# Kernel optimization log

Hardware: AMD Instinct MI355X
Metric: run time of the kernel (lower is better)

## Reference

```python
import jax, jax.numpy as jnp
import numpy as np

B = 4096        # batch_size
D = 256         # feature_dim
N = 9000000     # dataset size (state buffer length)
G = 100         # num_groups
ALPHA = 0.5     # alpha_weight
GAMMA = 0.8
RHO = 8.0
LAM = 1.0       # lambada
ETA_P = 0.01
EPS = 1e-14
CLIP = 5.0


def setup_inputs() -> dict:
    key = jax.random.key(0)
    k = jax.random.split(key, 6)
    zis = jax.random.normal(k[0], (B, D), jnp.float32)
    zjs = jax.random.normal(k[1], (B, D), jnp.float32)
    # per-sample learned temperatures, small positive values
    taus_I = 0.01 + 0.2 * jax.random.uniform(k[2], (N,), jnp.float32)
    taus_T = 0.01 + 0.2 * jax.random.uniform(k[3], (N,), jnp.float32)
    group_info_I = jax.random.randint(k[4], (N,), 0, G, dtype=jnp.int32)
    group_info_T = jax.random.randint(k[5], (N,), 0, G, dtype=jnp.int32)
    ids = jnp.arange(B, dtype=jnp.int32)  # unique sample indices
    zeros_N = jnp.zeros((N,), jnp.float32)
    return {
        "zis": zis, "zjs": zjs,
        "s_I": zeros_N, "s_T": zeros_N, "b_I": zeros_N, "b_T": zeros_N,
        "z_I": jnp.zeros((G,), jnp.float32), "z_T": jnp.zeros((G,), jnp.float32),
        "p_I": jnp.ones((G,), jnp.float32) / G, "p_T": jnp.ones((G,), jnp.float32) / G,
        "taus_I": taus_I, "taus_T": taus_T,
        "ids": ids, "group_info_I": group_info_I, "group_info_T": group_info_T,
    }


def _l2norm(x):
    return x / jnp.maximum(jnp.linalg.norm(x, axis=1, keepdims=True), 1e-12)


def reference(zis, zjs, s_I, s_T, b_I, b_T, z_I, z_T, p_I, p_T,
              taus_I, taus_T, ids, group_info_I, group_info_T):
    zis = _l2norm(zis)
    zjs = _l2norm(zjs)
    sim = zis @ zjs.T                                   # [B, B]
    diag = jnp.diagonal(sim)                            # [B]
    mask_neg = 1.0 - jnp.eye(B, dtype=sim.dtype)
    image_diffs = sim - diag[:, None]
    text_diffs = sim - diag[None, :]

    tau_I = taus_I[ids]                                 # [B]
    tau_T = taus_T[ids]
    idt = jax.lax.stop_gradient(image_diffs / tau_I[:, None])
    tdt = jax.lax.stop_gradient(text_diffs / tau_T[None, :])

    # running max state (numerically-stable exp)
    old_b_I = b_I[ids]
    b_I_new = jnp.maximum(jnp.max(idt, axis=1), old_b_I)    # [B]
    old_b_T = b_T[ids]
    b_T_new = jnp.maximum(jnp.max(tdt, axis=0), old_b_T)    # [B]
    b_I = b_I.at[ids].set(b_I_new)
    b_T = b_T.at[ids].set(b_T_new)

    exp_I = jnp.exp(idt - b_I_new[:, None]) * mask_neg
    exp_T = jnp.exp(tdt - b_T_new[None, :]) * mask_neg
    g_I = jnp.sum(exp_I, axis=1)                         # [B]
    g_T = jnp.sum(exp_T, axis=0)                         # [B]

    # EMA of softmax denominators with max-rescaling
    s_I_new = (1.0 - GAMMA) * s_I[ids] * jnp.exp(old_b_I - b_I_new) + GAMMA * g_I
    s_T_new = (1.0 - GAMMA) * s_T[ids] * jnp.exp(old_b_T - b_T_new) + GAMMA * g_T
    s_I = s_I.at[ids].set(s_I_new)
    s_T = s_T.at[ids].set(s_T_new)
    s_I_c = jnp.maximum(s_I_new, EPS)
    s_T_c = jnp.maximum(s_T_new, EPS)

    w_I = exp_I / s_I_c[:, None]
    w_T = exp_T / s_T_c[None, :]

    gid_I = group_info_I[ids]                            # [B]
    gid_T = group_info_T[ids]
    gw_I = G * p_I[gid_I]                                # [B]
    gw_T = G * p_T[gid_T]

    image_loss = jnp.sum(w_I * gw_I[:, None] * image_diffs, axis=1)   # [B]
    text_loss = jnp.sum(w_T * gw_T[None, :] * text_diffs, axis=0)     # [B]
    total_loss = ALPHA * image_loss.mean() + (1.0 - ALPHA) * text_loss.mean()

    # per-group adversarial weight update
    F_I = tau_I * (jnp.log(s_I_c) + b_I_new + RHO)       # [B]
    F_T = tau_T * (jnp.log(s_T_c) + b_T_new + RHO)
    ones_b = jnp.ones((B,), sim.dtype)
    cnt_I = jnp.maximum(jax.ops.segment_sum(ones_b, gid_I, num_segments=G), 1.0)
    cnt_T = jnp.maximum(jax.ops.segment_sum(ones_b, gid_T, num_segments=G), 1.0)
    grad_p_I = jax.ops.segment_sum(F_I, gid_I, num_segments=G) / cnt_I
    grad_p_T = jax.ops.segment_sum(F_T, gid_T, num_segments=G) / cnt_T

    z_I = (1.0 - GAMMA) * z_I + GAMMA * grad_p_I
    z_T = (1.0 - GAMMA) * z_T + GAMMA * grad_p_T
    grad_hp_I = -LAM * jnp.log(p_I + EPS) - LAM
    grad_hp_T = -LAM * jnp.log(p_T + EPS) - LAM
    new_p_I = p_I * jnp.exp(2.0 * ETA_P * jnp.clip(z_I + grad_hp_I, -CLIP, CLIP))
    new_p_T = p_T * jnp.exp(2.0 * ETA_P * jnp.clip(z_T + grad_hp_T, -CLIP, CLIP))
    p_I = new_p_I / new_p_I.sum()
    p_T = new_p_T / new_p_T.sum()

    return total_loss, p_I, p_T
```

## Files before the change

kernel.cpp:

```cpp
#include <hip/hip_runtime.h>
#include <hip/hip_bf16.h>
#include <math.h>

#define BB 4096
#define DD 256
#define GG 100
#define GAMMA_C 0.8f
#define RHO_C 8.0f
#define ALPHA_C 0.5f
#define EPS_C 1e-14f
#define NSR 64
#define NSC 32

typedef __bf16 bf16x8 __attribute__((ext_vector_type(8)));
typedef float f32x16 __attribute__((ext_vector_type(16)));

__device__ inline int swzLoc(int r31, int k) {
    return ((k >> 4) << 9) | (((((k >> 3) & 1) << 5) | r31) << 3) | (k & 7);
}

__device__ inline float blockReduceSum(float v, float* lds) {
    for (int o = 32; o > 0; o >>= 1) v += __shfl_down(v, o);
    int lane = threadIdx.x & 63, wid = threadIdx.x >> 6;
    if (lane == 0) lds[wid] = v;
    __syncthreads();
    if (threadIdx.x == 0) {
        float r = lds[0];
        int nw = blockDim.x >> 6;
        for (int w = 1; w < nw; w++) r += lds[w];
        lds[0] = r;
    }
    __syncthreads();
    float r = lds[0];
    __syncthreads();
    return r;
}

__global__ void __launch_bounds__(256) norm_kernel(const float* __restrict__ zis,
                            const float* __restrict__ zjs,
                            ushort* __restrict__ zhi, ushort* __restrict__ zlo,
                            ushort* __restrict__ whi, ushort* __restrict__ wlo,
                            float* __restrict__ diag, float* __restrict__ acc) {
    __shared__ ushort st[4][8192];
    int rb = blockIdx.x;
    int wv = threadIdx.x >> 6, lane = threadIdx.x & 63;
    if (rb == 0) { acc[threadIdx.x] = 0.f; acc[threadIdx.x + 256] = 0.f; }
    for (int rr = 0; rr < 8; rr++) {
        int r = rb * 32 + wv * 8 + rr;
        float4 zv = *(const float4*)&zis[r * DD + lane * 4];
        float4 wv4 = *(const float4*)&zjs[r * DD + lane * 4];
        float sz = zv.x * zv.x + zv.y * zv.y + zv.z * zv.z + zv.w * zv.w;
        float sw = wv4.x * wv4.x + wv4.y * wv4.y + wv4.z * wv4.z + wv4.w * wv4.w;
        float dt = zv.x * wv4.x + zv.y * wv4.y + zv.z * wv4.z + zv.w * wv4.w;
        for (int mask = 1; mask <= 32; mask <<= 1) {
            sz += __shfl_xor(sz, mask);
            sw += __shfl_xor(sw, mask);
            dt += __shfl_xor(dt, mask);
        }
        float iz = 1.0f / fmaxf(sqrtf(sz), 1e-12f);
        float iw = 1.0f / fmaxf(sqrtf(sw), 1e-12f);
        if (lane == 0) diag[r] = dt * iz * iw;
        float nz[4] = {zv.x * iz, zv.y * iz, zv.z * iz, zv.w * iz};
        float nw[4] = {wv4.x * iw, wv4.y * iw, wv4.z * iw, wv4.w * iw};
        int r31 = wv * 8 + rr;
        for (int e = 0; e < 4; e++) {
            int k = lane * 4 + e;
            int li = swzLoc(r31, k);
            __hip_bfloat16 hz = __float2bfloat16(nz[e]);
            __hip_bfloat16 lz = __float2bfloat16(nz[e] - __bfloat162float(hz));
            __hip_bfloat16 hw = __float2bfloat16(nw[e]);
            __hip_bfloat16 lw = __float2bfloat16(nw[e] - __bfloat162float(hw));
            st[0][li] = *(ushort*)&hz;
            st[1][li] = *(ushort*)&lz;
            st[2][li] = *(ushort*)&hw;
            st[3][li] = *(ushort*)&lw;
        }
    }
    __syncthreads();
    size_t base = (size_t)rb * 8192;
    ushort* dsts[4] = {zhi + base, zlo + base, whi + base, wlo + base};
    for (int a = 0; a < 4; a++) {
        uint4* d = (uint4*)dsts[a];
        const uint4* s = (const uint4*)st[a];
        for (int it = 0; it < 4; it++) {
            int idx = it * 256 + threadIdx.x;
            d[idx] = s[idx];
        }
    }
}

__global__ void __launch_bounds__(256, 4) fused_tile(const ushort* __restrict__ Ahi,
        const ushort* __restrict__ Alo, const ushort* __restrict__ Bhi,
        const ushort* __restrict__ Blo, const float* __restrict__ diag,
        const float* __restrict__ tausI, const float* __restrict__ tausT,
        const int* __restrict__ ids,
        float* __restrict__ pmR, float* __restrict__ pgR, float* __restrict__ pwR,
        float* __restrict__ pmC, float* __restrict__ pgC, float* __restrict__ pwC) {
    __shared__ float rDiag[128], rITau[128];
    __shared__ float cDiag[64], cITau[64];
    __shared__ float cmS[4][64], cgS[4][64], cwS[4][64];
    __shared__ float tr[4][32 * 65];

    int lane = threadIdx.x & 63;
    int wv = threadIdx.x >> 6;
    int bm = blockIdx.y * 128, bn = blockIdx.x * 64;
    int h = lane >> 5, cl = lane & 31;

    if (threadIdx.x < 128) {
        int r = bm + threadIdx.x;
        rDiag[threadIdx.x] = diag[r];
        rITau[threadIdx.x] = 1.0f / tausI[ids[r]];
    } else if (threadIdx.x < 192) {
        int c = bn + threadIdx.x - 128;
        cDiag[threadIdx.x - 128] = diag[c];
        cITau[threadIdx.x - 128] = 1.0f / tausT[ids[c]];
    }

    int aBase = (blockIdx.y * 4 + wv) * 8192;
    int b0 = (blockIdx.x * 2) * 8192;
    int b1 = b0 + 8192;
    int lofs = lane * 8;

    f32x16 acc[2] = {};
#pragma unroll
    for (int s = 0; s < 16; s++) {
        int so = s * 512 + lofs;
        bf16x8 ah  = *(const bf16x8*)&Ahi[aBase + so];
        bf16x8 al  = *(const bf16x8*)&Alo[aBase + so];
        bf16x8 bh0 = *(const bf16x8*)&Bhi[b0 + so];
        bf16x8 bl0 = *(const bf16x8*)&Blo[b0 + so];
        bf16x8 bh1 = *(const bf16x8*)&Bhi[b1 + so];
        bf16x8 bl1 = *(const bf16x8*)&Blo[b1 + so];
        acc[0] = __builtin_amdgcn_mfma_f32_32x32x16_bf16(ah, bh0, acc[0], 0, 0, 0);
        acc[1] = __builtin_amdgcn_mfma_f32_32x32x16_bf16(ah, bh1, acc[1], 0, 0, 0);
        acc[0] = __builtin_amdgcn_mfma_f32_32x32x16_bf16(ah, bl0, acc[0], 0, 0, 0);
        acc[1] = __builtin_amdgcn_mfma_f32_32x32x16_bf16(ah, bl1, acc[1], 0, 0, 0);
        acc[0] = __builtin_amdgcn_mfma_f32_32x32x16_bf16(al, bh0, acc[0], 0, 0, 0);
        acc[1] = __builtin_amdgcn_mfma_f32_32x32x16_bf16(al, bh1, acc[1], 0, 0, 0);
    }

    __syncthreads();
    float cd2[2], cit2[2], cbloc[2], cg[2] = {}, cw[2] = {};
#pragma unroll
    for (int u = 0; u < 2; u++) {
        int clc = u * 32 + cl;
        cd2[u] = cDiag[clc];
        cit2[u] = cITau[clc];
        float m = -INFINITY;
#pragma unroll
        for (int reg = 0; reg < 16; reg++) m = fmaxf(m, acc[u][reg]);
        m = fmaxf(m, __shfl_xor(m, 32));
        cbloc[u] = (m - cd2[u]) * cit2[u];
    }
#pragma unroll
    for (int u = 0; u < 2; u++) {
        int gc = bn + u * 32 + cl;
#pragma unroll
        for (int reg = 0; reg < 16; reg++) {
            int gr = bm + wv * 32 + (reg & 3) + 4 * h + 8 * (reg >> 2);
            float v = acc[u][reg];
            bool off = gr != gc;
            float dvT = v - cd2[u];
            float eT = off ? __expf(dvT * cit2[u] - cbloc[u]) : 0.f;
            cg[u] += eT;
            cw[u] += eT * dvT;
        }
    }
#pragma unroll
    for (int u = 0; u < 2; u++) {
        cg[u] += __shfl_xor(cg[u], 32);
        cw[u] += __shfl_xor(cw[u], 32);
        if (h == 0) {
            cmS[wv][u * 32 + cl] = cbloc[u];
            cgS[wv][u * 32 + cl] = cg[u];
            cwS[wv][u * 32 + cl] = cw[u];
        }
    }

#pragma unroll
    for (int u = 0; u < 2; u++)
#pragma unroll
        for (int reg = 0; reg < 16; reg++) {
            int r = (reg & 3) + 4 * h + 8 * (reg >> 2);
            tr[wv][r * 65 + u * 32 + cl] = acc[u][reg];
        }
    __syncthreads();

    if (threadIdx.x < 64) {
        int c = threadIdx.x;
        float m = fmaxf(fmaxf(cmS[0][c], cmS[1][c]), fmaxf(cmS[2][c], cmS[3][c]));
        float g = 0.f, w = 0.f;
        for (int wq = 0; wq < 4; wq++) {
            float f = __expf(cmS[wq][c] - m);
            g += cgS[wq][c] * f;
            w += cwS[wq][c] * f;
        }
        size_t o = (size_t)blockIdx.y * BB + bn + c;
        pmC[o] = m;
        pgC[o] = g;
        pwC[o] = w;
    }

    {
        int r = cl;
        int grow = bm + wv * 32 + r;
        float rd = rDiag[wv * 32 + r];
        float rit = rITau[wv * 32 + r];
        float vv[32];
#pragma unroll
        for (int j = 0; j < 32; j++) vv[j] = tr[wv][r * 65 + h * 32 + j];
        float m = -INFINITY;
#pragma unroll
        for (int j = 0; j < 32; j++) m = fmaxf(m, vv[j]);
        m = fmaxf(m, __shfl_xor(m, 32));
        float bloc = (m - rd) * rit;
        float rg = 0.f, rw = 0.f;
#pragma unroll
        for (int j = 0; j < 32; j++) {
            int gc = bn + h * 32 + j;
            float dv = vv[j] - rd;
            float e = (grow != gc) ? __expf(dv * rit - bloc) : 0.f;
            rg += e;
            rw += e * dv;
        }
        rg += __shfl_xor(rg, 32);
        rw += __shfl_xor(rw, 32);
        if (h == 0) {
            size_t o = (size_t)blockIdx.x * BB + grow;
            pmR[o] = bloc;
            pgR[o] = rg;
            pwR[o] = rw;
        }
    }
}

__global__ void __launch_bounds__(256) fin_kernel(
        const float* __restrict__ pmR, const float* __restrict__ pgR,
        const float* __restrict__ pwR, const float* __restrict__ pmC,
        const float* __restrict__ pgC, const float* __restrict__ pwC,
        const float* __restrict__ sI, const float* __restrict__ bI,
        const float* __restrict__ tausI, const int* __restrict__ gInfI,
        const float* __restrict__ pI,
        const float* __restrict__ sT, const float* __restrict__ bT,
        const float* __restrict__ tausT, const int* __restrict__ gInfT,
        const float* __restrict__ pT,
        const int* __restrict__ ids, float* __restrict__ acc,
        const float* __restrict__ zI, const float* __restrict__ zT,
        float* __restrict__ out) {
    __shared__ float lds[8];
    __shared__ float binF[GG], binC[GG];
    __shared__ float mS[4][64], gS[4][64], wS[4][64];
    __shared__ int lastFlag;
    if (threadIdx.x < GG) { binF[threadIdx.x] = 0.f; binC[threadIdx.x] = 0.f; }
    int side = blockIdx.x >> 6;
    int chunk = blockIdx.x & 63;
    int il = threadIdx.x & 63;
    int sg = threadIdx.x >> 6;
    int i = chunk * 64 + il;
    int ns = side ? NSC : NSR;
    const float* pm = side ? pmC : pmR;
    const float* pg = side ? pgC : pgR;
    const float* pw = side ? pwC : pwR;
    const float* sS = side ? sT : sI;
    const float* bS = side ? bT : bI;
    const float* taus = side ? tausT : tausI;
    const int* ginfo = side ? gInfT : gInfI;
    const float* pP = side ? pT : pI;

    float m = -INFINITY, g = 0.f, w = 0.f;
    for (int s = sg; s < ns; s += 4) {
        float pms = pm[(size_t)s * BB + i];
        float pgs = pg[(size_t)s * BB + i];
        float pws = pw[(size_t)s * BB + i];
        float mn = fmaxf(m, pms);
        float fo = __expf(m - mn);
        float fs = __expf(pms - mn);
        g = g * fo + pgs * fs;
        w = w * fo + pws * fs;
        m = mn;
    }
    mS[sg][il] = m;
    gS[sg][il] = g;
    wS[sg][il] = w;
    __syncthreads();

    float loss = 0.f;
    if (sg == 0) {
        int id = ids[i];
        float oldb = bS[id];
        float mm = fmaxf(fmaxf(mS[0][il], mS[1][il]), fmaxf(mS[2][il], mS[3][il]));
        float bfin = fmaxf(mm, oldb);
        float gg2 = 0.f, ww2 = 0.f;
        for (int q = 0; q < 4; q++) {
            float f = __expf(mS[q][il] - bfin);
            gg2 += gS[q][il] * f;
            ww2 += wS[q][il] * f;
        }
        float tau = taus[id];
        float snew = (1.f - GAMMA_C) * sS[id] * expf(oldb - bfin) + GAMMA_C * gg2;
        float sc = fmaxf(snew, EPS_C);
        int gid = ginfo[id];
        float gw = (float)GG * pP[gid];
        loss = gw * ww2 / sc;
        float F = tau * (logf(sc) + bfin + RHO_C);
        atomicAdd(&binF[gid], F);
        atomicAdd(&binC[gid], 1.0f);
    }
    float lsum = blockReduceSum(loss, lds);
    if (threadIdx.x == 0) atomicAdd(&acc[side], lsum);
    __syncthreads();
    if (threadIdx.x < GG) {
        atomicAdd(&acc[2 + side * 200 + threadIdx.x], binF[threadIdx.x]);
        atomicAdd(&acc[102 + side * 200 + threadIdx.x], binC[threadIdx.x]);
    }

    __threadfence();
    if (threadIdx.x == 0) {
        int old = atomicAdd((int*)&acc[408], 1);
        lastFlag = (old == 127);
    }
    __syncthreads();
    if (!lastFlag) return;

    int gg = threadIdx.x;
    float npI = 0.f, npT = 0.f;
    if (gg < GG) {
        float cI = __hip_atomic_load(&acc[102 + gg], __ATOMIC_RELAXED, __HIP_MEMORY_SCOPE_AGENT);
        float fI = __hip_atomic_load(&acc[2 + gg], __ATOMIC_RELAXED, __HIP_MEMORY_SCOPE_AGENT);
        float gpI = fI / fmaxf(cI, 1.f);
        float zi = (1.f - GAMMA_C) * zI[gg] + GAMMA_C * gpI;
        float ghpI = -logf(pI[gg] + EPS_C) - 1.f;
        float ti = fminf(fmaxf(zi + ghpI, -5.f), 5.f);
        npI = pI[gg] * expf(0.02f * ti);

        float cT = __hip_atomic_load(&acc[302 + gg], __ATOMIC_RELAXED, __HIP_MEMORY_SCOPE_AGENT);
        float fT = __hip_atomic_load(&acc[202 + gg], __ATOMIC_RELAXED, __HIP_MEMORY_SCOPE_AGENT);
        float gpT = fT / fmaxf(cT, 1.f);
        float zt = (1.f - GAMMA_C) * zT[gg] + GAMMA_C * gpT;
        float ghpT = -logf(pT[gg] + EPS_C) - 1.f;
        float tt = fminf(fmaxf(zt + ghpT, -5.f), 5.f);
        npT = pT[gg] * expf(0.02f * tt);
    }
    float sumI = blockReduceSum(npI, lds);
    float sumT = blockReduceSum(npT, lds);
    if (gg < GG) {
        out[1 + gg] = npI / sumI;
        out[101 + gg] = npT / sumT;
    }
    if (gg == 0) {
        float lI = __hip_atomic_load(&acc[0], __ATOMIC_RELAXED, __HIP_MEMORY_SCOPE_AGENT);
        float lT = __hip_atomic_load(&acc[1], __ATOMIC_RELAXED, __HIP_MEMORY_SCOPE_AGENT);
        out[0] = ALPHA_C * (lI / (float)BB) + (1.f - ALPHA_C) * (lT / (float)BB);
    }
}

extern "C" void kernel_launch(void* const* d_in, const int* in_sizes, int n_in,
                              void* d_out, int out_size, void* d_ws, size_t ws_size,
                              hipStream_t stream) {
    const float* zis   = (const float*)d_in[0];
    const float* zjs   = (const float*)d_in[1];
    const float* s_I   = (const float*)d_in[2];
    const float* s_T   = (const float*)d_in[3];
    const float* b_I   = (const float*)d_in[4];
    const float* b_T   = (const float*)d_in[5];
    const float* z_I   = (const float*)d_in[6];
    const float* z_T   = (const float*)d_in[7];
    const float* p_I   = (const float*)d_in[8];
    const float* p_T   = (const float*)d_in[9];
    const float* tausI = (const float*)d_in[10];
    const float* tausT = (const float*)d_in[11];
    const int*   ids   = (const int*)d_in[12];
    const int*   gInfI = (const int*)d_in[13];
    const int*   gInfT = (const int*)d_in[14];
    float* out = (float*)d_out;

    char* ws = (char*)d_ws;
    ushort* zhi = (ushort*)ws;
    ushort* zlo = zhi + (size_t)BB * DD;
    ushort* whi = zlo + (size_t)BB * DD;
    ushort* wlo = whi + (size_t)BB * DD;
    float* acc  = (float*)(wlo + (size_t)BB * DD);
    float* diag = acc + 512;
    float* pmR  = diag + BB;
    float* pgR  = pmR + (size_t)NSR * BB;
    float* pwR  = pgR + (size_t)NSR * BB;
    float* pmC  = pwR + (size_t)NSR * BB;
    float* pgC  = pmC + (size_t)NSC * BB;
    float* pwC  = pgC + (size_t)NSC * BB;

    norm_kernel<<<128, 256, 0, stream>>>(zis, zjs, zhi, zlo, whi, wlo, diag, acc);
    fused_tile<<<dim3(64, 32), 256, 0, stream>>>(zhi, zlo, whi, wlo, diag,
            tausI, tausT, ids, pmR, pgR, pwR, pmC, pgC, pwC);
    fin_kernel<<<128, 256, 0, stream>>>(pmR, pgR, pwR, pmC, pgC, pwC,
            s_I, b_I, tausI, gInfI, p_I, s_T, b_T, tausT, gInfT, p_T, ids, acc,
            z_I, z_T, out);
}
```

Baseline: 270.2 us.

## Halve row-transpose LDS buffer, raise occupancy, and widen finalize grid

The fused tile kernel now transposes accumulators through a half-size LDS buffer in two passes of 16 rows. Each row's 64 columns are split across four lanes and combined with extra shuffles, and launch bounds are raised from 4 to 6 waves per SIMD. The aim is lower LDS and register use so more blocks fit per CU. The finalize kernel is relaunched with 256 blocks of 32 rows each and 8 stripe groups per block, spreading the partial-reduction reads over more parallel work. The trade-off is extra shuffles and syncs, plus possible register spills under the tighter bound.

```diff
diff --git a/kernel.cpp b/kernel.cpp
--- a/kernel.cpp
+++ b/kernel.cpp
@@ -89,7 +89,7 @@
     }
 }
 
-__global__ void __launch_bounds__(256, 4) fused_tile(const ushort* __restrict__ Ahi,
+__global__ void __launch_bounds__(256, 6) fused_tile(const ushort* __restrict__ Ahi,
         const ushort* __restrict__ Alo, const ushort* __restrict__ Bhi,
         const ushort* __restrict__ Blo, const float* __restrict__ diag,
         const float* __restrict__ tausI, const float* __restrict__ tausT,
@@ -99,7 +99,7 @@
     __shared__ float rDiag[128], rITau[128];
     __shared__ float cDiag[64], cITau[64];
     __shared__ float cmS[4][64], cgS[4][64], cwS[4][64];
-    __shared__ float tr[4][32 * 65];
+    __shared__ float tr16[4][16 * 65];
 
     int lane = threadIdx.x & 63;
     int wv = threadIdx.x >> 6;
@@ -176,14 +176,6 @@
             cwS[wv][u * 32 + cl] = cw[u];
         }
     }
-
-#pragma unroll
-    for (int u = 0; u < 2; u++)
-#pragma unroll
-        for (int reg = 0; reg < 16; reg++) {
-            int r = (reg & 3) + 4 * h + 8 * (reg >> 2);
-            tr[wv][r * 65 + u * 32 + cl] = acc[u][reg];
-        }
     __syncthreads();
 
     if (threadIdx.x < 64) {
@@ -201,32 +193,46 @@
         pwC[o] = w;
     }
 
-    {
-        int r = cl;
-        int grow = bm + wv * 32 + r;
-        float rd = rDiag[wv * 32 + r];
-        float rit = rITau[wv * 32 + r];
-        float vv[32];
-#pragma unroll
-        for (int j = 0; j < 32; j++) vv[j] = tr[wv][r * 65 + h * 32 + j];
+    int stripeR = blockIdx.x;
+#pragma unroll
+    for (int hf = 0; hf < 2; hf++) {
+#pragma unroll
+        for (int u = 0; u < 2; u++)
+#pragma unroll
+            for (int rr = 0; rr < 8; rr++) {
+                int r = (rr & 3) + 4 * h + 8 * (rr >> 2);
+                tr16[wv][r * 65 + u * 32 + cl] = acc[u][hf * 8 + rr];
+            }
+        int row = cl & 15;
+        int q = (h << 1) | (cl >> 4);
+        int rl = wv * 32 + hf * 16 + row;
+        int grow = bm + rl;
+        float rd = rDiag[rl];
+        float rit = rITau[rl];
+        float vv[16];
+#pragma unroll
+        for (int j = 0; j < 16; j++) vv[j] = tr16[wv][row * 65 + q * 16 + j];
         float m = -INFINITY;
 #pragma unroll
-        for (int j = 0; j < 32; j++) m = fmaxf(m, vv[j]);
+        for (int j = 0; j < 16; j++) m = fmaxf(m, vv[j]);
+        m = fmaxf(m, __shfl_xor(m, 16));
         m = fmaxf(m, __shfl_xor(m, 32));
         float bloc = (m - rd) * rit;
         float rg = 0.f, rw = 0.f;
 #pragma unroll
-        for (int j = 0; j < 32; j++) {
-            int gc = bn + h * 32 + j;
+        for (int j = 0; j < 16; j++) {
+            int gc = bn + q * 16 + j;
             float dv = vv[j] - rd;
             float e = (grow != gc) ? __expf(dv * rit - bloc) : 0.f;
             rg += e;
             rw += e * dv;
         }
+        rg += __shfl_xor(rg, 16);
         rg += __shfl_xor(rg, 32);
+        rw += __shfl_xor(rw, 16);
         rw += __shfl_xor(rw, 32);
-        if (h == 0) {
-            size_t o = (size_t)blockIdx.x * BB + grow;
+        if ((lane & 48) == 0) {
+            size_t o = (size_t)stripeR * BB + grow;
             pmR[o] = bloc;
             pgR[o] = rg;
             pwR[o] = rw;
@@ -249,14 +255,14 @@
         float* __restrict__ out) {
     __shared__ float lds[8];
     __shared__ float binF[GG], binC[GG];
-    __shared__ float mS[4][64], gS[4][64], wS[4][64];
+    __shared__ float mS[8][32], gS[8][32], wS[8][32];
     __shared__ int lastFlag;
     if (threadIdx.x < GG) { binF[threadIdx.x] = 0.f; binC[threadIdx.x] = 0.f; }
-    int side = blockIdx.x >> 6;
-    int chunk = blockIdx.x & 63;
-    int il = threadIdx.x & 63;
-    int sg = threadIdx.x >> 6;
-    int i = chunk * 64 + il;
+    int side = blockIdx.x >> 7;
+    int chunk = blockIdx.x & 127;
+    int il = threadIdx.x & 31;
+    int sg = threadIdx.x >> 5;
+    int i = chunk * 32 + il;
     int ns = side ? NSC : NSR;
     const float* pm = side ? pmC : pmR;
     const float* pg = side ? pgC : pgR;
@@ -268,7 +274,7 @@
     const float* pP = side ? pT : pI;
 
     float m = -INFINITY, g = 0.f, w = 0.f;
-    for (int s = sg; s < ns; s += 4) {
+    for (int s = sg; s < ns; s += 8) {
         float pms = pm[(size_t)s * BB + i];
         float pgs = pg[(size_t)s * BB + i];
         float pws = pw[(size_t)s * BB + i];
@@ -288,10 +294,11 @@
     if (sg == 0) {
         int id = ids[i];
         float oldb = bS[id];
-        float mm = fmaxf(fmaxf(mS[0][il], mS[1][il]), fmaxf(mS[2][il], mS[3][il]));
+        float mm = mS[0][il];
+        for (int q = 1; q < 8; q++) mm = fmaxf(mm, mS[q][il]);
         float bfin = fmaxf(mm, oldb);
         float gg2 = 0.f, ww2 = 0.f;
-        for (int q = 0; q < 4; q++) {
+        for (int q = 0; q < 8; q++) {
             float f = __expf(mS[q][il] - bfin);
             gg2 += gS[q][il] * f;
             ww2 += wS[q][il] * f;
@@ -317,7 +324,7 @@
     __threadfence();
     if (threadIdx.x == 0) {
         int old = atomicAdd((int*)&acc[408], 1);
-        lastFlag = (old == 127);
+        lastFlag = (old == 255);
     }
     __syncthreads();
     if (!lastFlag) return;
@@ -391,7 +398,7 @@
     norm_kernel<<<128, 256, 0, stream>>>(zis, zjs, zhi, zlo, whi, wlo, diag, acc);
     fused_tile<<<dim3(64, 32), 256, 0, stream>>>(zhi, zlo, whi, wlo, diag,
             tausI, tausT, ids, pmR, pgR, pwR, pmC, pgC, pwC);
-    fin_kernel<<<128, 256, 0, stream>>>(pmR, pgR, pwR, pmC, pgC, pwC,
+    fin_kernel<<<256, 256, 0, stream>>>(pmR, pgR, pwR, pmC, pgC, pwC,
             s_I, b_I, tausI, gInfI, p_I, s_T, b_T, tausT, gInfT, p_T, ids, acc,
             z_I, z_T, out);
 }
```

Result: slower. 277.3 us (+2.6%).
